# Kernel tuning notes

Measured on AMD Instinct MI355X. Metric: run time of the kernel, lower is better.

## Reference

```python
import jax, jax.numpy as jnp
from jax import lax
import numpy as np

DN = ('NCHW', 'OIHW', 'NCHW')

def _conv(x, w, b, s, p):
    out = lax.conv_general_dilated(x, w, (s, s), ((p, p), (p, p)), dimension_numbers=DN)
    return out + b[None, :, None, None]

def _convt(x, w, b):
    # torch ConvTranspose2d(k=3, stride=2, pad=1, out_pad=1) == lhs-dilated conv
    # with flipped kernel, pad (k-1-p, k-1-p+op) = (1, 2). Doubles H, W.
    wk = jnp.flip(w, (2, 3)).transpose(1, 0, 2, 3)  # [Cin,Cout,k,k] -> [Cout,Cin,k,k]
    out = lax.conv_general_dilated(x, wk, (1, 1), ((1, 2), (1, 2)), lhs_dilation=(2, 2), dimension_numbers=DN)
    return out + b[None, :, None, None]

def _bn(x, g, b):
    # training-mode batch stats over (N, H, W), eps=1e-5
    m = jnp.mean(x, (0, 2, 3), keepdims=True)
    v = jnp.var(x, (0, 2, 3), keepdims=True)
    return (x - m) * lax.rsqrt(v + 1e-5) * g[None, :, None, None] + b[None, :, None, None]

def _hsw(x):
    return x * jnp.clip(x + 3.0, 0.0, 6.0) * (1.0 / 6.0)

SCORE_THRESHOLD = 0.6
DOWN_SCALE = 4.0

def _forward(feature, ch_w1, ch_b1, ch_w2, ch_b2, ch_w3, ch_b3, ch_g1, ch_be1, ch_g2, ch_be2,
             cl_w1, cl_b1, cl_w2, cl_b2, cl_g, cl_be, cl_dw, cl_db,
             rg_tw, rg_tb, rg_g, rg_be, rg_w, rg_b, hm_tw, hm_tb):
    # ---- CommonHead (note: original reuses bn1 after both stride-2 convs) ----
    h = _bn(_conv(feature, ch_w1, ch_b1, 2, 1), ch_g1, ch_be1)   # [B,192,64,64]
    h = _bn(_conv(h, ch_w2, ch_b2, 2, 1), ch_g1, ch_be1)         # [B,192,32,32]
    h = _hsw(_bn(_conv(h, ch_w3, ch_b3, 1, 0), ch_g2, ch_be2))   # [B,32,32,32]
    # ---- PageClassifyNet ----
    c = _hsw(_bn(_conv(h, cl_w1, cl_b1, 1, 1), cl_g, cl_be))     # [B,32,32,32]
    c = _conv(c, cl_w2, cl_b2, 1, 1)                             # [B,1,32,32]
    cls = c.reshape(c.shape[0], -1) @ cl_dw.T + cl_db            # [B,2]
    r = _hsw(_bn(_convt(feature, rg_tw, rg_tb), rg_g, rg_be))    # [B,32,256,256]
    reg = _conv(r, rg_w, rg_b, 1, 1)                             # [B,2,256,256]
    # ---- AuxiliaryHeatmapNet ----
    hm = _convt(feature, hm_tw, hm_tb)                           # [B,8,256,256]
    # ---- keypoint decode (threshold + argmax + gather), vectorized over batch ----
    B, _, H, W = hm.shape
    flat = hm.transpose(0, 2, 3, 1).reshape(B, H * W, 8)          # HWC layout as in source
    pages = jnp.stack([flat[..., :4], flat[..., 4:]], axis=1)     # [B,2(pages),HW,4(corners)]
    idx = jnp.argmax(pages, axis=2)                               # [B,2,4] flat spatial index
    y_idx = (idx // W).astype(reg.dtype)
    x_idx = (idx % W).astype(reg.dtype)
    fi = idx.reshape(B, -1)                                       # [B,8]
    reg_flat = reg.reshape(B, 2, H * W)
    off_x = jnp.take_along_axis(reg_flat[:, 0, :], fi, axis=1).reshape(B, 2, 4)
    off_y = jnp.take_along_axis(reg_flat[:, 1, :], fi, axis=1).reshape(B, 2, 4)
    xs = jnp.clip((off_x + x_idx) * DOWN_SCALE / (W * DOWN_SCALE), 0.0, 1.0)
    ys = jnp.clip((off_y + y_idx) * DOWN_SCALE / (H * DOWN_SCALE), 0.0, 1.0)
    valid = cls > SCORE_THRESHOLD                                 # [B,2]
    label = jnp.broadcast_to(jnp.arange(2, dtype=xs.dtype)[None, :], (B, 2))
    row = jnp.concatenate([label[..., None], xs, ys], axis=-1)    # [B,2,9]
    return jnp.where(valid[..., None], row, jnp.asarray(-1.0, xs.dtype))


def setup_inputs() -> dict:
    key = jax.random.key(0)
    ks = jax.random.split(key, 32)
    rn = lambda k, shp, s=0.05: jax.random.normal(k, shp, dtype=jnp.float32) * s
    d = {}
    d['feature'] = jax.random.normal(ks[0], (8, 512, 128, 128), dtype=jnp.float32)
    d['ch_w1'] = rn(ks[1], (192, 512, 3, 3)); d['ch_b1'] = rn(ks[2], (192,))
    d['ch_w2'] = rn(ks[3], (192, 192, 3, 3)); d['ch_b2'] = rn(ks[4], (192,))
    d['ch_w3'] = rn(ks[5], (32, 192, 1, 1)); d['ch_b3'] = rn(ks[6], (32,))
    d['ch_g1'] = jnp.ones((192,), jnp.float32); d['ch_be1'] = jnp.zeros((192,), jnp.float32)
    d['ch_g2'] = jnp.ones((32,), jnp.float32); d['ch_be2'] = jnp.zeros((32,), jnp.float32)
    d['cl_w1'] = rn(ks[7], (32, 32, 3, 3)); d['cl_b1'] = rn(ks[8], (32,))
    d['cl_w2'] = rn(ks[9], (1, 32, 3, 3)); d['cl_b2'] = rn(ks[10], (1,))
    d['cl_g'] = jnp.ones((32,), jnp.float32); d['cl_be'] = jnp.zeros((32,), jnp.float32)
    d['cl_dw'] = rn(ks[11], (2, 1024), 0.1); d['cl_db'] = rn(ks[12], (2,))
    d['rg_tw'] = rn(ks[13], (512, 32, 3, 3)); d['rg_tb'] = rn(ks[14], (32,))
    d['rg_g'] = jnp.ones((32,), jnp.float32); d['rg_be'] = jnp.zeros((32,), jnp.float32)
    d['rg_w'] = rn(ks[15], (2, 32, 3, 3)); d['rg_b'] = rn(ks[16], (2,))
    d['hm_tw'] = rn(ks[17], (512, 8, 3, 3)); d['hm_tb'] = rn(ks[18], (8,))
    return d


def reference(feature, ch_w1, ch_b1, ch_w2, ch_b2, ch_w3, ch_b3, ch_g1, ch_be1, ch_g2, ch_be2,
              cl_w1, cl_b1, cl_w2, cl_b2, cl_g, cl_be, cl_dw, cl_db,
              rg_tw, rg_tb, rg_g, rg_be, rg_w, rg_b, hm_tw, hm_tb):
    return _forward(feature, ch_w1, ch_b1, ch_w2, ch_b2, ch_w3, ch_b3, ch_g1, ch_be1, ch_g2, ch_be2,
                    cl_w1, cl_b1, cl_w2, cl_b2, cl_g, cl_be, cl_dw, cl_db,
                    rg_tw, rg_tb, rg_g, rg_be, rg_w, rg_b, hm_tw, hm_tb)
```

## Files before the change

### kernel.cpp

```cpp
#include <hip/hip_runtime.h>

typedef unsigned short u16;
typedef u16 u16x8 __attribute__((ext_vector_type(8)));
typedef __bf16 bf16x8 __attribute__((ext_vector_type(8)));
typedef float f32x4 __attribute__((ext_vector_type(4)));

__device__ __forceinline__ float bf2f(u16 v) {
  unsigned u = ((unsigned)v) << 16;
  return __builtin_bit_cast(float, u);
}
__device__ __forceinline__ u16 f2bf(float f) {
  unsigned u = __builtin_bit_cast(unsigned, f);
  u += 0x7FFFu + ((u >> 16) & 1u);
  return (u16)(u >> 16);
}
__device__ __forceinline__ float hsw(float v) {
  return v * fminf(fmaxf(v + 3.f, 0.f), 6.f) * (1.f / 6.f);
}
__device__ __forceinline__ f32x4 mfma16(u16x8 a, u16x8 b, f32x4 c) {
  return __builtin_amdgcn_mfma_f32_16x16x32_bf16(
      __builtin_bit_cast(bf16x8, a), __builtin_bit_cast(bf16x8, b), c, 0, 0, 0);
}

#define LR 40

__global__ __launch_bounds__(256) void k_tobf(const float* __restrict__ f,
                                              u16* __restrict__ fbh) {
  __shared__ float tl[64 * 65];
  const int t = threadIdx.x;
  const int bid = blockIdx.x;
  const int ict = bid & 7, xt = (bid >> 3) & 1, y = (bid >> 4) & 127, n = bid >> 11;
  const int x0 = xt * 64, ic0 = ict * 64;
#pragma unroll
  for (int i = 0; i < 16; ++i) {
    const int e = t + i * 256;
    const int icl = e >> 6, xl = e & 63;
    tl[icl * 65 + xl] = f[((n * 512 + ic0 + icl) * 128 + y) * 128 + x0 + xl];
  }
  __syncthreads();
#pragma unroll
  for (int i = 0; i < 16; ++i) {
    const int e = t + i * 256;
    const int xl = e >> 6, icl = e & 63;
    const size_t idx = ((size_t)((n * 128 + y) * 128 + x0 + xl) << 9) + ic0 + icl;
    fbh[idx] = f2bf(tl[icl * 65 + xl]);
  }
}

__global__ __launch_bounds__(256) void k_pack1(const float* __restrict__ w,
                                               u16* __restrict__ bph) {
  const int e = blockIdx.x * 256 + threadIdx.x;
  const int ici = e & 31;
  const int rest = e >> 5;
  const int oc = rest % 192;
  const int kc = rest / 192;
  const int icc = kc & 15, tap = kc >> 4;
  const int ic = icc * 32 + ici;
  bph[e] = f2bf(w[(oc * 512 + ic) * 9 + tap]);
}

__global__ __launch_bounds__(256) void k_pack2(const float* __restrict__ w,
                                               u16* __restrict__ bph) {
  const int e = blockIdx.x * 256 + threadIdx.x;
  const int ici = e & 31;
  const int rest = e >> 5;
  const int oc = rest % 192;
  const int kc = rest / 192;
  const int icc = kc % 6, tap = kc / 6;
  const int ic = icc * 32 + ici;
  bph[e] = f2bf(w[(oc * 192 + ic) * 9 + tap]);
}

__global__ __launch_bounds__(256) void k_pack5(const float* __restrict__ rgw,
                                               const float* __restrict__ hmw,
                                               u16* __restrict__ bph) {
  const int e = blockIdx.x * 256 + threadIdx.x;
  const int ici = e & 31;
  const int rest = e >> 5;
  const int oc = rest % 48;
  const int sic = rest / 48;
  const int icc = sic & 15, slot = sic >> 4;
  const int ic = icc * 32 + ici;
  const int kytab[9] = {1, 1, 1, 2, 0, 2, 2, 0, 0};
  const int kxtab[9] = {1, 2, 0, 1, 1, 2, 0, 2, 0};
  const int ky = kytab[slot], kx = kxtab[slot];
  float v = 0.f;
  if (oc < 32)
    v = rgw[((ic * 32 + oc) * 3 + ky) * 3 + kx];
  else if (oc < 40)
    v = hmw[((ic * 8 + (oc - 32)) * 3 + ky) * 3 + kx];
  bph[e] = f2bf(v);
}

__global__ __launch_bounds__(256) void k_conv1(const u16* __restrict__ fbh,
                                               const u16* __restrict__ bph,
                                               const float* __restrict__ bias,
                                               float* __restrict__ y1) {
  __shared__ u16 Al[64 * LR];
  __shared__ u16 Bl[192 * LR];
  __shared__ float bl[192];
  const int t = threadIdx.x;
  const int n = blockIdx.x >> 6, oy = blockIdx.x & 63;
  if (t < 192) bl[t] = bias[t];
  const int lane = t & 63, wv = t >> 6;
  const int row = lane & 15, g = lane >> 4;
  const int oxs = t >> 2, icq = t & 3;
  const f32x4 z4 = {0.f, 0.f, 0.f, 0.f};
  f32x4 acc[4][3];
#pragma unroll
  for (int i = 0; i < 4; ++i)
#pragma unroll
    for (int j = 0; j < 3; ++j) acc[i][j] = z4;

  for (int kc = 0; kc < 144; ++kc) {
    const int tap = kc >> 4, icc = kc & 15;
    const int ky = tap / 3, kx = tap - ky * 3;
    const int iy = 2 * oy - 1 + ky;
    const int ix = 2 * oxs - 1 + kx;
    u16x8 av = {0, 0, 0, 0, 0, 0, 0, 0};
    if ((unsigned)iy < 128u && (unsigned)ix < 128u)
      av = *(const u16x8*)&fbh[((size_t)((n * 128 + iy) * 128 + ix) << 9) +
                               icc * 32 + icq * 8];
    u16x8 bv[3];
    const size_t bbase = (size_t)(tap * 16 + icc) * (192 * 32);
#pragma unroll
    for (int i = 0; i < 3; ++i) {
      const int e = t + i * 256;
      bv[i] = *(const u16x8*)&bph[bbase + (e >> 2) * 32 + (e & 3) * 8];
    }
    __syncthreads();
    *(u16x8*)&Al[oxs * LR + icq * 8] = av;
#pragma unroll
    for (int i = 0; i < 3; ++i) {
      const int e = t + i * 256;
      *(u16x8*)&Bl[(e >> 2) * LR + (e & 3) * 8] = bv[i];
    }
    __syncthreads();
    u16x8 af[4], bf[3];
#pragma unroll
    for (int mf = 0; mf < 4; ++mf)
      af[mf] = *(const u16x8*)&Al[(mf * 16 + row) * LR + g * 8];
#pragma unroll
    for (int nf = 0; nf < 3; ++nf)
      bf[nf] = *(const u16x8*)&Bl[(wv * 48 + nf * 16 + row) * LR + g * 8];
#pragma unroll
    for (int mf = 0; mf < 4; ++mf)
#pragma unroll
      for (int nf = 0; nf < 3; ++nf) acc[mf][nf] = mfma16(af[mf], bf[nf], acc[mf][nf]);
  }
#pragma unroll
  for (int mf = 0; mf < 4; ++mf)
#pragma unroll
    for (int nf = 0; nf < 3; ++nf)
#pragma unroll
      for (int r = 0; r < 4; ++r) {
        const int m = mf * 16 + g * 4 + r;
        const int oc = wv * 48 + nf * 16 + row;
        y1[((n * 64 + oy) * 64 + m) * 192 + oc] = acc[mf][nf][r] + bl[oc];
      }
}

__global__ __launch_bounds__(256) void k_conv2(const float* __restrict__ y1,
                                               const u16* __restrict__ bph,
                                               const float* __restrict__ bias,
                                               const float* __restrict__ sc,
                                               const float* __restrict__ sh,
                                               float* __restrict__ y2) {
  __shared__ u16 Al[64 * LR];
  __shared__ u16 Bl[192 * LR];
  __shared__ float bl[192], scl[192], shl[192];
  const int t = threadIdx.x;
  const int n = blockIdx.x >> 4, oyp = blockIdx.x & 15;
  if (t < 192) {
    bl[t] = bias[t];
    scl[t] = sc[t];
    shl[t] = sh[t];
  }
  __syncthreads();
  const int lane = t & 63, wv = t >> 6;
  const int row = lane & 15, g = lane >> 4;
  const int ms = t >> 2, icq = t & 3;
  const int ryr = ms >> 5, oxs = ms & 31;
  const f32x4 z4 = {0.f, 0.f, 0.f, 0.f};
  f32x4 acc[4][3];
#pragma unroll
  for (int i = 0; i < 4; ++i)
#pragma unroll
    for (int j = 0; j < 3; ++j) acc[i][j] = z4;

  for (int kc = 0; kc < 54; ++kc) {
    const int tap = kc / 6, icc = kc - tap * 6;
    const int ky = tap / 3, kx = tap - ky * 3;
    const int iy = 2 * (oyp * 2 + ryr) - 1 + ky;
    const int ix = 2 * oxs - 1 + kx;
    u16x8 av = {0, 0, 0, 0, 0, 0, 0, 0};
    if ((unsigned)iy < 64u && (unsigned)ix < 64u) {
      const int icb = icc * 32 + icq * 8;
      const float* base = &y1[((n * 64 + iy) * 64 + ix) * 192 + icb];
      const f32x4 r0 = *(const f32x4*)base;
      const f32x4 r1 = *(const f32x4*)(base + 4);
#pragma unroll
      for (int j = 0; j < 8; ++j) {
        const float r = (j < 4) ? r0[j & 3] : r1[j & 3];
        av[j] = f2bf(r * scl[icb + j] + shl[icb + j]);
      }
    }
    u16x8 bv[3];
    const size_t bbase = (size_t)(tap * 6 + icc) * (192 * 32);
#pragma unroll
    for (int i = 0; i < 3; ++i) {
      const int e = t + i * 256;
      bv[i] = *(const u16x8*)&bph[bbase + (e >> 2) * 32 + (e & 3) * 8];
    }
    __syncthreads();
    *(u16x8*)&Al[ms * LR + icq * 8] = av;
#pragma unroll
    for (int i = 0; i < 3; ++i) {
      const int e = t + i * 256;
      *(u16x8*)&Bl[(e >> 2) * LR + (e & 3) * 8] = bv[i];
    }
    __syncthreads();
    u16x8 af[4], bf[3];
#pragma unroll
    for (int mf = 0; mf < 4; ++mf)
      af[mf] = *(const u16x8*)&Al[(mf * 16 + row) * LR + g * 8];
#pragma unroll
    for (int nf = 0; nf < 3; ++nf)
      bf[nf] = *(const u16x8*)&Bl[(wv * 48 + nf * 16 + row) * LR + g * 8];
#pragma unroll
    for (int mf = 0; mf < 4; ++mf)
#pragma unroll
      for (int nf = 0; nf < 3; ++nf) acc[mf][nf] = mfma16(af[mf], bf[nf], acc[mf][nf]);
  }
#pragma unroll
  for (int mf = 0; mf < 4; ++mf)
#pragma unroll
    for (int nf = 0; nf < 3; ++nf)
#pragma unroll
      for (int r = 0; r < 4; ++r) {
        const int m = mf * 16 + g * 4 + r;
        const int oy = oyp * 2 + (m >> 5), ox = m & 31;
        const int oc = wv * 48 + nf * 16 + row;
        y2[((n * 32 + oy) * 32 + ox) * 192 + oc] = acc[mf][nf][r] + bl[oc];
      }
}

#define AST 40
#define ARS (130 * 40)
#define BST 40
__global__ __launch_bounds__(256) void k_convt(const u16* __restrict__ fbh,
                                               const u16* __restrict__ bph,
                                               const float* __restrict__ rgb,
                                               const float* __restrict__ hmb,
                                               u16* __restrict__ rr,
                                               float* __restrict__ hm) {
  __shared__ u16 AH[2 * ARS];
  __shared__ u16 BH[9 * 48 * BST];
  const int t = threadIdx.x;
  const int bid = (blockIdx.x & 7) * 128 + (blockIdx.x >> 3);
  const int n = bid >> 7, iyb = bid & 127;
  const int lane = t & 63, wv = t >> 6;
  const int row = lane & 15, g = lane >> 4;

  if (t < 8) {
    const int r = t >> 2, j = t & 3;
    const u16x8 z = {0, 0, 0, 0, 0, 0, 0, 0};
    *(u16x8*)&AH[r * ARS + 128 * AST + j * 8] = z;
  }

  float bias3[3];
#pragma unroll
  for (int nf = 0; nf < 3; ++nf) {
    const int oc = nf * 16 + row;
    bias3[nf] = (oc < 32) ? rgb[oc] : ((oc < 40) ? hmb[oc - 32] : 0.f);
  }

  const int SCt[9] = {0, 1, 1, 2, 2, 3, 3, 3, 3};
  const int SDt[9] = {0, 0, 0, 0, 1, 0, 0, 1, 1};
  const int SXt[9] = {0, 0, 1, 0, 0, 0, 1, 0, 1};

  int rr_[4], px_[4], iq_[4];
#pragma unroll
  for (int i = 0; i < 4; ++i) {
    const int u = t + i * 256;
    rr_[i] = u >> 9;
    px_[i] = (u >> 2) & 127;
    iq_[i] = u & 3;
  }

  const f32x4 z4 = {0.f, 0.f, 0.f, 0.f};
  f32x4 acc[4][2][3];
#pragma unroll
  for (int c = 0; c < 4; ++c)
#pragma unroll
    for (int m = 0; m < 2; ++m)
#pragma unroll
      for (int j = 0; j < 3; ++j) acc[c][m][j] = z4;

#define LOAD_A(ICC, DST)                                                       \
  _Pragma("unroll") for (int i = 0; i < 4; ++i) {                              \
    const int iy = iyb + rr_[i];                                               \
    u16x8 v = {0, 0, 0, 0, 0, 0, 0, 0};                                        \
    if (iy < 128)                                                              \
      v = *(const u16x8*)&fbh[((size_t)((n * 128 + iy) * 128 + px_[i]) << 9) + \
                              (ICC)*32 + iq_[i] * 8];                          \
    DST[i] = v;                                                                \
  }

#define LOAD_B(ICC, DST)                                                       \
  _Pragma("unroll") for (int i = 0; i < 7; ++i) {                              \
    const int e = t + i * 256;                                                 \
    u16x8 v = {0, 0, 0, 0, 0, 0, 0, 0};                                        \
    if (e < 1728) {                                                            \
      const int slot = e / 192, rem = e % 192;                                 \
      const int oc = rem >> 2, icq = rem & 3;                                  \
      v = *(const u16x8*)&bph[((size_t)((slot * 16 + (ICC)) * 48 + oc) << 5) + \
                              icq * 8];                                        \
    }                                                                          \
    DST[i] = v;                                                                \
  }

  u16x8 ahA[4], bhA[7], ahB[4], bhB[7];
  LOAD_A(0, ahA);
  LOAD_B(0, bhA);

  for (int icc = 0; icc < 16; ++icc) {
    __syncthreads();
#pragma unroll
    for (int i = 0; i < 4; ++i)
      *(u16x8*)&AH[rr_[i] * ARS + px_[i] * AST + iq_[i] * 8] = ahA[i];
#pragma unroll
    for (int i = 0; i < 7; ++i) {
      const int e = t + i * 256;
      if (e < 1728) {
        const int slot = e / 192, rem = e % 192;
        const int oc = rem >> 2, icq = rem & 3;
        *(u16x8*)&BH[(slot * 48 + oc) * BST + icq * 8] = bhA[i];
      }
    }
    __syncthreads();

    if (icc < 15) {
      LOAD_A(icc + 1, ahB);
      LOAD_B(icc + 1, bhB);
    }

#pragma unroll
    for (int slot = 0; slot < 9; ++slot) {
      const int cls = SCt[slot], diy = SDt[slot], dix = SXt[slot];
      const u16x8 bf0 = *(const u16x8*)&BH[(slot * 48 + row) * BST + g * 8];
      const u16x8 bf1 = *(const u16x8*)&BH[(slot * 48 + 16 + row) * BST + g * 8];
      const u16x8 bf2 = *(const u16x8*)&BH[(slot * 48 + 32 + row) * BST + g * 8];
#pragma unroll
      for (int mfl = 0; mfl < 2; ++mfl) {
        const int mf = wv * 2 + mfl;
        const u16x8 af =
            *(const u16x8*)&AH[diy * ARS + (mf * 16 + row + dix) * AST + g * 8];
        acc[cls][mfl][0] = mfma16(af, bf0, acc[cls][mfl][0]);
        acc[cls][mfl][1] = mfma16(af, bf1, acc[cls][mfl][1]);
        acc[cls][mfl][2] = mfma16(af, bf2, acc[cls][mfl][2]);
      }
    }

#pragma unroll
    for (int i = 0; i < 4; ++i) ahA[i] = ahB[i];
#pragma unroll
    for (int i = 0; i < 7; ++i) bhA[i] = bhB[i];
  }
#undef LOAD_A
#undef LOAD_B

#pragma unroll
  for (int cls = 0; cls < 4; ++cls) {
    const int oy = 2 * iyb + (cls >> 1);
    const int xp = cls & 1;
#pragma unroll
    for (int mfl = 0; mfl < 2; ++mfl)
#pragma unroll
      for (int nf = 0; nf < 3; ++nf)
#pragma unroll
        for (int r = 0; r < 4; ++r) {
          const int m = (wv * 2 + mfl) * 16 + g * 4 + r;
          const int ox = 2 * m + xp;
          const int oc = nf * 16 + row;
          const float v = acc[cls][mfl][nf][r] + bias3[nf];
          if (oc < 32)
            rr[((size_t)((n * 256 + oy) * 256 + ox)) * 32 + oc] = f2bf(v);
          else if (oc < 40)
            hm[(size_t)(n * 8 + (oc - 32)) * 65536 + oy * 256 + ox] = v;
        }
  }
}

template <int CG, bool BF16>
__global__ __launch_bounds__(256) void k_stats(const void* __restrict__ in_, int M,
                                               int PB, float* __restrict__ gsum,
                                               float* __restrict__ gsq) {
  const int C = CG * 32;
  __shared__ float red[8][CG * 32];
  const int t = threadIdx.x;
  const int pg = t >> 5, ln = t & 31;
  float s[CG], q[CG];
#pragma unroll
  for (int c = 0; c < CG; ++c) { s[c] = 0.f; q[c] = 0.f; }
  const int p0 = blockIdx.x * PB;
  const int pend = min(p0 + PB, M);
  for (int p = p0 + pg; p < pend; p += 8) {
#pragma unroll
    for (int c = 0; c < CG; ++c) {
      float v;
      if (BF16)
        v = bf2f(((const u16*)in_)[(size_t)p * C + c * 32 + ln]);
      else
        v = ((const float*)in_)[(size_t)p * C + c * 32 + ln];
      s[c] += v;
      q[c] += v * v;
    }
  }
#pragma unroll
  for (int c = 0; c < CG; ++c) red[pg][c * 32 + ln] = s[c];
  __syncthreads();
  if (t < C) {
    float tot = 0.f;
#pragma unroll
    for (int k = 0; k < 8; ++k) tot += red[k][t];
    atomicAdd(&gsum[t], tot);
  }
  __syncthreads();
#pragma unroll
  for (int c = 0; c < CG; ++c) red[pg][c * 32 + ln] = q[c];
  __syncthreads();
  if (t < C) {
    float tot = 0.f;
#pragma unroll
    for (int k = 0; k < 8; ++k) tot += red[k][t];
    atomicAdd(&gsq[t], tot);
  }
}

__global__ void k_bnfin(const float* __restrict__ gsum, const float* __restrict__ gsq,
                        const float* __restrict__ g, const float* __restrict__ be,
                        float invM, int C, float* __restrict__ sc,
                        float* __restrict__ sh) {
  const int t = threadIdx.x;
  if (t < C) {
    const float m = gsum[t] * invM;
    const float var = gsq[t] * invM - m * m;
    const float inv = rsqrtf(var + 1e-5f);
    const float s = g[t] * inv;
    sc[t] = s;
    sh[t] = be[t] - m * s;
  }
}

__global__ __launch_bounds__(256) void k_conv3(const float* __restrict__ y2,
                                               const float* __restrict__ w3,
                                               const float* __restrict__ b3,
                                               const float* __restrict__ sc,
                                               const float* __restrict__ sh,
                                               float* __restrict__ y3) {
  __shared__ float wl[32 * 192];
  __shared__ float scl[192], shl[192];
  const int t = threadIdx.x;
  for (int e = t; e < 6144; e += 256) wl[e] = w3[e];
  if (t < 192) {
    scl[t] = sc[t];
    shl[t] = sh[t];
  }
  __syncthreads();
  const int px = blockIdx.x * 256 + t;
  float acc[32];
#pragma unroll
  for (int oc = 0; oc < 32; ++oc) acc[oc] = 0.f;
  const float* base = &y2[(size_t)px * 192];
  for (int icb = 0; icb < 192; icb += 8) {
    const f32x4 r0 = *(const f32x4*)&base[icb];
    const f32x4 r1 = *(const f32x4*)&base[icb + 4];
    float v[8];
#pragma unroll
    for (int j = 0; j < 8; ++j) {
      const float r = (j < 4) ? r0[j & 3] : r1[j & 3];
      v[j] = r * scl[icb + j] + shl[icb + j];
    }
#pragma unroll
    for (int oc = 0; oc < 32; ++oc) {
      const f32x4 w0 = *(const f32x4*)&wl[oc * 192 + icb];
      const f32x4 w1 = *(const f32x4*)&wl[oc * 192 + icb + 4];
      acc[oc] += v[0] * w0[0] + v[1] * w0[1] + v[2] * w0[2] + v[3] * w0[3] +
                 v[4] * w1[0] + v[5] * w1[1] + v[6] * w1[2] + v[7] * w1[3];
    }
  }
#pragma unroll
  for (int oc = 0; oc < 32; ++oc) y3[(size_t)px * 32 + oc] = acc[oc] + b3[oc];
}

__global__ __launch_bounds__(256) void k_clsconv1(const float* __restrict__ y3,
                                                  const float* __restrict__ w1,
                                                  const float* __restrict__ b1,
                                                  const float* __restrict__ sc,
                                                  const float* __restrict__ sh,
                                                  float* __restrict__ c1) {
  __shared__ float wl[9216];
  __shared__ float scl[32], shl[32];
  const int t = threadIdx.x;
  for (int e = t; e < 9216; e += 256) {
    const int oc = e & 31;
    const int tmp = e >> 5;
    const int tap = tmp % 9, ic = tmp / 9;
    wl[e] = w1[(oc * 32 + ic) * 9 + tap];
  }
  if (t < 32) {
    scl[t] = sc[t];
    shl[t] = sh[t];
  }
  __syncthreads();
  const int px = blockIdx.x * 64 + (t & 63);
  const int ocg = t >> 6;
  const int n = px >> 10, y0 = (px >> 5) & 31, x0 = px & 31;
  float acc[8];
#pragma unroll
  for (int j = 0; j < 8; ++j) acc[j] = 0.f;
  for (int tap = 0; tap < 9; ++tap) {
    const int dy = tap / 3 - 1, dx = tap % 3 - 1;
    const int yy = y0 + dy, xx = x0 + dx;
    if ((unsigned)yy < 32u && (unsigned)xx < 32u) {
      const float* ib = &y3[((n << 10) + yy * 32 + xx) * 32];
      for (int ic = 0; ic < 32; ++ic) {
        const float v = hsw(ib[ic] * scl[ic] + shl[ic]);
        const float* wp = &wl[(ic * 9 + tap) * 32 + ocg * 8];
#pragma unroll
        for (int j = 0; j < 8; ++j) acc[j] += v * wp[j];
      }
    }
  }
#pragma unroll
  for (int j = 0; j < 8; ++j) c1[px * 32 + ocg * 8 + j] = acc[j] + b1[ocg * 8 + j];
}

__global__ __launch_bounds__(256) void k_cls(const float* __restrict__ c1,
                                             const float* __restrict__ w2,
                                             const float* __restrict__ b2,
                                             const float* __restrict__ dw,
                                             const float* __restrict__ db,
                                             const float* __restrict__ sc,
                                             const float* __restrict__ sh,
                                             float* __restrict__ cls) {
  __shared__ float wl[288];
  __shared__ float scl[32], shl[32];
  __shared__ float red0[256], red1[256];
  const int t = threadIdx.x;
  const int n = blockIdx.x;
  for (int e = t; e < 288; e += 256) wl[e] = w2[e];
  if (t < 32) {
    scl[t] = sc[t];
    shl[t] = sh[t];
  }
  __syncthreads();
  float s0 = 0.f, s1 = 0.f;
  for (int i = 0; i < 4; ++i) {
    const int px = i * 256 + t;
    const int y0 = px >> 5, x0 = px & 31;
    float c2 = b2[0];
    for (int tap = 0; tap < 9; ++tap) {
      const int dy = tap / 3 - 1, dx = tap % 3 - 1;
      const int yy = y0 + dy, xx = x0 + dx;
      if ((unsigned)yy < 32u && (unsigned)xx < 32u) {
        const float* ib = &c1[((n << 10) + yy * 32 + xx) * 32];
        for (int ic = 0; ic < 32; ++ic)
          c2 += hsw(ib[ic] * scl[ic] + shl[ic]) * wl[ic * 9 + tap];
      }
    }
    s0 += c2 * dw[px];
    s1 += c2 * dw[1024 + px];
  }
  red0[t] = s0;
  red1[t] = s1;
  __syncthreads();
  for (int s = 128; s; s >>= 1) {
    if (t < s) {
      red0[t] += red0[t + s];
      red1[t] += red1[t + s];
    }
    __syncthreads();
  }
  if (t == 0) {
    cls[n * 2 + 0] = red0[0] + db[0];
    cls[n * 2 + 1] = red1[0] + db[1];
  }
}

__global__ __launch_bounds__(256) void k_regconv(const u16* __restrict__ rr,
                                                 const float* __restrict__ w,
                                                 const float* __restrict__ b,
                                                 const float* __restrict__ sc,
                                                 const float* __restrict__ sh,
                                                 float* __restrict__ reg) {
  __shared__ u16 rl[3 * 258 * 33];
  __shared__ float wl[576];
  __shared__ float scl[32], shl[32];
  const int t = threadIdx.x;
  const int n = blockIdx.x >> 8, oy = blockIdx.x & 255;
  for (int e = t; e < 576; e += 256) wl[e] = w[e];
  if (t < 32) {
    scl[t] = sc[t];
    shl[t] = sh[t];
  }
  if (t < 192) {
    const int ry = t / 64, side = (t >> 5) & 1, ic = t & 31;
    rl[(ry * 258 + side * 257) * 33 + ic] = 0;
  }
  __syncthreads();
  for (int e = t; e < 3072; e += 256) {
    const int icq8 = e & 3;
    const int pxx = (e >> 2) & 255;
    const int ry = e >> 10;
    const int rowi = oy - 1 + ry;
    u16x8 raw = {0, 0, 0, 0, 0, 0, 0, 0};
    bool ok = (unsigned)rowi < 256u;
    if (ok)
      raw = *(const u16x8*)&rr[((size_t)((n * 256 + rowi) * 256 + pxx)) * 32 + icq8 * 8];
#pragma unroll
    for (int j = 0; j < 8; ++j) {
      const int ic = icq8 * 8 + j;
      float v = 0.f;
      if (ok) v = hsw(bf2f(raw[j]) * scl[ic] + shl[ic]);
      rl[(ry * 258 + pxx + 1) * 33 + ic] = f2bf(v);
    }
  }
  __syncthreads();
  const int px = t;
  float a0 = b[0], a1 = b[1];
#pragma unroll
  for (int ry = 0; ry < 3; ++ry)
#pragma unroll
    for (int kx = 0; kx < 3; ++kx) {
      const u16* ib = &rl[(ry * 258 + px + kx) * 33];
      for (int ic = 0; ic < 32; ++ic) {
        const float v = bf2f(ib[ic]);
        a0 += v * wl[ic * 9 + ry * 3 + kx];
        a1 += v * wl[288 + ic * 9 + ry * 3 + kx];
      }
    }
  reg[(n * 2 + 0) * 65536 + oy * 256 + px] = a0;
  reg[(n * 2 + 1) * 65536 + oy * 256 + px] = a1;
}

__global__ __launch_bounds__(256) void k_argmax(const float* __restrict__ hm,
                                                int* __restrict__ idx) {
  __shared__ float bv[256];
  __shared__ int bi[256];
  const int t = threadIdx.x;
  const float* base = &hm[(size_t)blockIdx.x * 65536];
  float best = -3.402823466e38f;
  int bidx = 2147483647;
  for (int i = t; i < 65536; i += 256) {
    const float v = base[i];
    if (v > best) {
      best = v;
      bidx = i;
    }
  }
  bv[t] = best;
  bi[t] = bidx;
  __syncthreads();
  for (int s = 128; s; s >>= 1) {
    if (t < s) {
      if (bv[t + s] > bv[t] || (bv[t + s] == bv[t] && bi[t + s] < bi[t])) {
        bv[t] = bv[t + s];
        bi[t] = bi[t + s];
      }
    }
    __syncthreads();
  }
  if (t == 0) idx[blockIdx.x] = bi[0];
}

__global__ void k_final(const float* __restrict__ cls, const int* __restrict__ idx,
                        const float* __restrict__ reg, float* __restrict__ out) {
  const int t = threadIdx.x;
  if (t >= 16) return;
  const int n = t >> 1, p = t & 1;
  const float cv = cls[n * 2 + p];
  float* o = &out[(n * 2 + p) * 9];
  if (!(cv > 0.6f)) {
    for (int i = 0; i < 9; ++i) o[i] = -1.f;
    return;
  }
  o[0] = (float)p;
  for (int c = 0; c < 4; ++c) {
    const int id = idx[n * 8 + p * 4 + c];
    const int yi = id >> 8, xi = id & 255;
    const float ox_ = reg[(n * 2 + 0) * 65536 + id];
    const float oy_ = reg[(n * 2 + 1) * 65536 + id];
    o[1 + c] = fminf(fmaxf((ox_ + (float)xi) * (1.f / 256.f), 0.f), 1.f);
    o[5 + c] = fminf(fmaxf((oy_ + (float)yi) * (1.f / 256.f), 0.f), 1.f);
  }
}

extern "C" void kernel_launch(void* const* d_in, const int* in_sizes, int n_in,
                              void* d_out, int out_size, void* d_ws, size_t ws_size,
                              hipStream_t stream) {
  const float* feature = (const float*)d_in[0];
  const float* ch_w1 = (const float*)d_in[1];
  const float* ch_b1 = (const float*)d_in[2];
  const float* ch_w2 = (const float*)d_in[3];
  const float* ch_b2 = (const float*)d_in[4];
  const float* ch_w3 = (const float*)d_in[5];
  const float* ch_b3 = (const float*)d_in[6];
  const float* ch_g1 = (const float*)d_in[7];
  const float* ch_be1 = (const float*)d_in[8];
  const float* ch_g2 = (const float*)d_in[9];
  const float* ch_be2 = (const float*)d_in[10];
  const float* cl_w1 = (const float*)d_in[11];
  const float* cl_b1 = (const float*)d_in[12];
  const float* cl_w2 = (const float*)d_in[13];
  const float* cl_b2 = (const float*)d_in[14];
  const float* cl_g = (const float*)d_in[15];
  const float* cl_be = (const float*)d_in[16];
  const float* cl_dw = (const float*)d_in[17];
  const float* cl_db = (const float*)d_in[18];
  const float* rg_tw = (const float*)d_in[19];
  const float* rg_tb = (const float*)d_in[20];
  const float* rg_g = (const float*)d_in[21];
  const float* rg_be = (const float*)d_in[22];
  const float* rg_w = (const float*)d_in[23];
  const float* rg_b = (const float*)d_in[24];
  const float* hm_tw = (const float*)d_in[25];
  const float* hm_tb = (const float*)d_in[26];
  float* out = (float*)d_out;

  char* w = (char*)d_ws;
  const size_t OFF_FB = 0;
  const size_t OFF_BP1 = 134217728;
  const size_t OFF_BP2 = 135987200;
  const size_t OFF_BP5 = 136650752;
  const size_t OFF_Y1 = 137093120;
  const size_t OFF_Y2 = 162258944;
  const size_t OFF_Y3 = 168550400;
  const size_t OFF_C1 = 169598976;
  const size_t OFF_RR = 170647552;
  const size_t OFF_HM = 204201984;
  const size_t OFF_REG = 220979200;
  const size_t OFF_STATS = 225173504;
  const size_t OFF_PARAMS = 225177344;
  const size_t OFF_CLS = 225181184;
  const size_t OFF_IDX = 225181248;
  const size_t WS_NEED = 225181504;
  if (ws_size < WS_NEED) return;

  u16* FB = (u16*)(w + OFF_FB);
  u16* BP1 = (u16*)(w + OFF_BP1);
  u16* BP2 = (u16*)(w + OFF_BP2);
  u16* BP5 = (u16*)(w + OFF_BP5);
  float* Y1 = (float*)(w + OFF_Y1);
  float* Y2 = (float*)(w + OFF_Y2);
  float* Y3 = (float*)(w + OFF_Y3);
  float* C1 = (float*)(w + OFF_C1);
  u16* RR = (u16*)(w + OFF_RR);
  float* HM = (float*)(w + OFF_HM);
  float* REG = (float*)(w + OFF_REG);
  float* GSUM = (float*)(w + OFF_STATS);
  float* GSQ = GSUM + 480;
  float* SC = (float*)(w + OFF_PARAMS);
  float* SH = SC + 480;
  float* CLS = (float*)(w + OFF_CLS);
  int* IDX = (int*)(w + OFF_IDX);

  (void)hipMemsetAsync(w + OFF_STATS, 0, 3840, stream);

  k_tobf<<<16384, 256, 0, stream>>>(feature, FB);
  k_pack1<<<3456, 256, 0, stream>>>(ch_w1, BP1);
  k_pack2<<<1296, 256, 0, stream>>>(ch_w2, BP2);
  k_pack5<<<864, 256, 0, stream>>>(rg_tw, hm_tw, BP5);

  k_conv1<<<512, 256, 0, stream>>>(FB, BP1, ch_b1, Y1);
  k_stats<6, false><<<128, 256, 0, stream>>>(Y1, 32768, 256, GSUM + 0, GSQ + 0);
  k_bnfin<<<1, 256, 0, stream>>>(GSUM + 0, GSQ + 0, ch_g1, ch_be1, 1.f / 32768.f, 192,
                                 SC + 0, SH + 0);
  k_conv2<<<128, 256, 0, stream>>>(Y1, BP2, ch_b2, SC + 0, SH + 0, Y2);
  k_stats<6, false><<<32, 256, 0, stream>>>(Y2, 8192, 256, GSUM + 192, GSQ + 192);
  k_bnfin<<<1, 256, 0, stream>>>(GSUM + 192, GSQ + 192, ch_g1, ch_be1, 1.f / 8192.f,
                                 192, SC + 192, SH + 192);
  k_conv3<<<32, 256, 0, stream>>>(Y2, ch_w3, ch_b3, SC + 192, SH + 192, Y3);
  k_stats<1, false><<<8, 256, 0, stream>>>(Y3, 8192, 1024, GSUM + 384, GSQ + 384);
  k_bnfin<<<1, 256, 0, stream>>>(GSUM + 384, GSQ + 384, ch_g2, ch_be2, 1.f / 8192.f,
                                 32, SC + 384, SH + 384);
  k_clsconv1<<<128, 256, 0, stream>>>(Y3, cl_w1, cl_b1, SC + 384, SH + 384, C1);
  k_stats<1, false><<<8, 256, 0, stream>>>(C1, 8192, 1024, GSUM + 416, GSQ + 416);
  k_bnfin<<<1, 256, 0, stream>>>(GSUM + 416, GSQ + 416, cl_g, cl_be, 1.f / 8192.f, 32,
                                 SC + 416, SH + 416);
  k_cls<<<8, 256, 0, stream>>>(C1, cl_w2, cl_b2, cl_dw, cl_db, SC + 416, SH + 416,
                               CLS);
  k_convt<<<1024, 256, 0, stream>>>(FB, BP5, rg_tb, hm_tb, RR, HM);
  k_stats<1, true><<<256, 256, 0, stream>>>(RR, 524288, 2048, GSUM + 448, GSQ + 448);
  k_bnfin<<<1, 256, 0, stream>>>(GSUM + 448, GSQ + 448, rg_g, rg_be, 1.f / 524288.f,
                                 32, SC + 448, SH + 448);
  k_regconv<<<2048, 256, 0, stream>>>(RR, rg_w, rg_b, SC + 448, SH + 448, REG);
  k_argmax<<<64, 256, 0, stream>>>(HM, IDX);
  k_final<<<1, 64, 0, stream>>>(CLS, IDX, REG, out);
}
```

Before: 836.3 us.

## Prefetch next K-chunk in conv1/conv2, store Y1 as bf16, retune convt LDS

conv1 and conv2 now issue global loads for the next K-chunk into registers before running the MFMAs on the current chunk, so load latency overlaps compute. The conv1 output Y1 is stored as bf16 instead of fp32, which halves its write and read traffic in conv1, the stats pass and conv2. The convt kernel drops the LDS row padding from 40 to 32 elements and hoists its A-fragment loads out of the slot loop. In exchange, the unpadded stride may cause LDS bank conflicts, the extra registers may lower occupancy, and BN statistics are now computed on bf16-rounded values.

```diff
diff --git a/kernel.cpp b/kernel.cpp
--- a/kernel.cpp
+++ b/kernel.cpp
@@ -95,7 +95,7 @@
 __global__ __launch_bounds__(256) void k_conv1(const u16* __restrict__ fbh,
                                                const u16* __restrict__ bph,
                                                const float* __restrict__ bias,
-                                               float* __restrict__ y1) {
+                                               u16* __restrict__ y1) {
   __shared__ u16 Al[64 * LR];
   __shared__ u16 Bl[192 * LR];
   __shared__ float bl[192];
@@ -112,30 +112,37 @@
 #pragma unroll
     for (int j = 0; j < 3; ++j) acc[i][j] = z4;
 
+#define C1_LOAD(KC, AV, BV)                                                    \
+  {                                                                            \
+    const int tap_ = (KC) >> 4, icc_ = (KC)&15;                                \
+    const int ky_ = tap_ / 3, kx_ = tap_ - ky_ * 3;                            \
+    const int iy_ = 2 * oy - 1 + ky_;                                          \
+    const int ix_ = 2 * oxs - 1 + kx_;                                         \
+    u16x8 v_ = {0, 0, 0, 0, 0, 0, 0, 0};                                       \
+    if ((unsigned)iy_ < 128u && (unsigned)ix_ < 128u)                          \
+      v_ = *(const u16x8*)&fbh[((size_t)((n * 128 + iy_) * 128 + ix_) << 9) +  \
+                               icc_ * 32 + icq * 8];                           \
+    AV = v_;                                                                   \
+    const size_t bbase_ = (size_t)(tap_ * 16 + icc_) * (192 * 32);             \
+    _Pragma("unroll") for (int i_ = 0; i_ < 3; ++i_) {                         \
+      const int e_ = t + i_ * 256;                                             \
+      BV[i_] = *(const u16x8*)&bph[bbase_ + (e_ >> 2) * 32 + (e_ & 3) * 8];    \
+    }                                                                          \
+  }
+
+  u16x8 avA, bvA[3], avB, bvB[3];
+  C1_LOAD(0, avA, bvA);
+
   for (int kc = 0; kc < 144; ++kc) {
-    const int tap = kc >> 4, icc = kc & 15;
-    const int ky = tap / 3, kx = tap - ky * 3;
-    const int iy = 2 * oy - 1 + ky;
-    const int ix = 2 * oxs - 1 + kx;
-    u16x8 av = {0, 0, 0, 0, 0, 0, 0, 0};
-    if ((unsigned)iy < 128u && (unsigned)ix < 128u)
-      av = *(const u16x8*)&fbh[((size_t)((n * 128 + iy) * 128 + ix) << 9) +
-                               icc * 32 + icq * 8];
-    u16x8 bv[3];
-    const size_t bbase = (size_t)(tap * 16 + icc) * (192 * 32);
+    __syncthreads();
+    *(u16x8*)&Al[oxs * LR + icq * 8] = avA;
 #pragma unroll
     for (int i = 0; i < 3; ++i) {
       const int e = t + i * 256;
-      bv[i] = *(const u16x8*)&bph[bbase + (e >> 2) * 32 + (e & 3) * 8];
+      *(u16x8*)&Bl[(e >> 2) * LR + (e & 3) * 8] = bvA[i];
     }
     __syncthreads();
-    *(u16x8*)&Al[oxs * LR + icq * 8] = av;
-#pragma unroll
-    for (int i = 0; i < 3; ++i) {
-      const int e = t + i * 256;
-      *(u16x8*)&Bl[(e >> 2) * LR + (e & 3) * 8] = bv[i];
-    }
-    __syncthreads();
+    if (kc < 143) C1_LOAD(kc + 1, avB, bvB);
     u16x8 af[4], bf[3];
 #pragma unroll
     for (int mf = 0; mf < 4; ++mf)
@@ -147,7 +154,11 @@
     for (int mf = 0; mf < 4; ++mf)
 #pragma unroll
       for (int nf = 0; nf < 3; ++nf) acc[mf][nf] = mfma16(af[mf], bf[nf], acc[mf][nf]);
-  }
+    avA = avB;
+#pragma unroll
+    for (int i = 0; i < 3; ++i) bvA[i] = bvB[i];
+  }
+#undef C1_LOAD
 #pragma unroll
   for (int mf = 0; mf < 4; ++mf)
 #pragma unroll
@@ -156,11 +167,11 @@
       for (int r = 0; r < 4; ++r) {
         const int m = mf * 16 + g * 4 + r;
         const int oc = wv * 48 + nf * 16 + row;
-        y1[((n * 64 + oy) * 64 + m) * 192 + oc] = acc[mf][nf][r] + bl[oc];
+        y1[((n * 64 + oy) * 64 + m) * 192 + oc] = f2bf(acc[mf][nf][r] + bl[oc]);
       }
 }
 
-__global__ __launch_bounds__(256) void k_conv2(const float* __restrict__ y1,
+__global__ __launch_bounds__(256) void k_conv2(const u16* __restrict__ y1,
                                                const u16* __restrict__ bph,
                                                const float* __restrict__ bias,
                                                const float* __restrict__ sc,
@@ -188,38 +199,47 @@
 #pragma unroll
     for (int j = 0; j < 3; ++j) acc[i][j] = z4;
 
+#define C2_LOAD(KC, RAW, OK, BV)                                               \
+  {                                                                            \
+    const int tap_ = (KC) / 6, icc_ = (KC)-tap_ * 6;                           \
+    const int ky_ = tap_ / 3, kx_ = tap_ - ky_ * 3;                            \
+    const int iy_ = 2 * (oyp * 2 + ryr) - 1 + ky_;                             \
+    const int ix_ = 2 * oxs - 1 + kx_;                                         \
+    OK = ((unsigned)iy_ < 64u) && ((unsigned)ix_ < 64u);                       \
+    u16x8 v_ = {0, 0, 0, 0, 0, 0, 0, 0};                                       \
+    if (OK)                                                                    \
+      v_ = *(const u16x8*)&y1[((n * 64 + iy_) * 64 + ix_) * 192 + icc_ * 32 +  \
+                              icq * 8];                                        \
+    RAW = v_;                                                                  \
+    const size_t bbase_ = (size_t)(tap_ * 6 + icc_) * (192 * 32);              \
+    _Pragma("unroll") for (int i_ = 0; i_ < 3; ++i_) {                         \
+      const int e_ = t + i_ * 256;                                             \
+      BV[i_] = *(const u16x8*)&bph[bbase_ + (e_ >> 2) * 32 + (e_ & 3) * 8];    \
+    }                                                                          \
+  }
+
+  u16x8 rawA, bvA[3], rawB, bvB[3];
+  bool okA, okB;
+  C2_LOAD(0, rawA, okA, bvA);
+
   for (int kc = 0; kc < 54; ++kc) {
     const int tap = kc / 6, icc = kc - tap * 6;
-    const int ky = tap / 3, kx = tap - ky * 3;
-    const int iy = 2 * (oyp * 2 + ryr) - 1 + ky;
-    const int ix = 2 * oxs - 1 + kx;
+    const int icb = icc * 32 + icq * 8;
     u16x8 av = {0, 0, 0, 0, 0, 0, 0, 0};
-    if ((unsigned)iy < 64u && (unsigned)ix < 64u) {
-      const int icb = icc * 32 + icq * 8;
-      const float* base = &y1[((n * 64 + iy) * 64 + ix) * 192 + icb];
-      const f32x4 r0 = *(const f32x4*)base;
-      const f32x4 r1 = *(const f32x4*)(base + 4);
-#pragma unroll
-      for (int j = 0; j < 8; ++j) {
-        const float r = (j < 4) ? r0[j & 3] : r1[j & 3];
-        av[j] = f2bf(r * scl[icb + j] + shl[icb + j]);
-      }
-    }
-    u16x8 bv[3];
-    const size_t bbase = (size_t)(tap * 6 + icc) * (192 * 32);
+    if (okA) {
+#pragma unroll
+      for (int j = 0; j < 8; ++j)
+        av[j] = f2bf(bf2f(rawA[j]) * scl[icb + j] + shl[icb + j]);
+    }
+    __syncthreads();
+    *(u16x8*)&Al[ms * LR + icq * 8] = av;
 #pragma unroll
     for (int i = 0; i < 3; ++i) {
       const int e = t + i * 256;
-      bv[i] = *(const u16x8*)&bph[bbase + (e >> 2) * 32 + (e & 3) * 8];
+      *(u16x8*)&Bl[(e >> 2) * LR + (e & 3) * 8] = bvA[i];
     }
     __syncthreads();
-    *(u16x8*)&Al[ms * LR + icq * 8] = av;
-#pragma unroll
-    for (int i = 0; i < 3; ++i) {
-      const int e = t + i * 256;
-      *(u16x8*)&Bl[(e >> 2) * LR + (e & 3) * 8] = bv[i];
-    }
-    __syncthreads();
+    if (kc < 53) C2_LOAD(kc + 1, rawB, okB, bvB);
     u16x8 af[4], bf[3];
 #pragma unroll
     for (int mf = 0; mf < 4; ++mf)
@@ -231,7 +251,12 @@
     for (int mf = 0; mf < 4; ++mf)
 #pragma unroll
       for (int nf = 0; nf < 3; ++nf) acc[mf][nf] = mfma16(af[mf], bf[nf], acc[mf][nf]);
-  }
+    rawA = rawB;
+    okA = okB;
+#pragma unroll
+    for (int i = 0; i < 3; ++i) bvA[i] = bvB[i];
+  }
+#undef C2_LOAD
 #pragma unroll
   for (int mf = 0; mf < 4; ++mf)
 #pragma unroll
@@ -245,17 +270,16 @@
       }
 }
 
-#define AST 40
-#define ARS (130 * 40)
-#define BST 40
+#define AST2 32
+#define ARS2 (129 * 32)
 __global__ __launch_bounds__(256) void k_convt(const u16* __restrict__ fbh,
                                                const u16* __restrict__ bph,
                                                const float* __restrict__ rgb,
                                                const float* __restrict__ hmb,
                                                u16* __restrict__ rr,
                                                float* __restrict__ hm) {
-  __shared__ u16 AH[2 * ARS];
-  __shared__ u16 BH[9 * 48 * BST];
+  __shared__ u16 AH[2 * ARS2];
+  __shared__ u16 BH[9 * 48 * 32];
   const int t = threadIdx.x;
   const int bid = (blockIdx.x & 7) * 128 + (blockIdx.x >> 3);
   const int n = bid >> 7, iyb = bid & 127;
@@ -265,7 +289,7 @@
   if (t < 8) {
     const int r = t >> 2, j = t & 3;
     const u16x8 z = {0, 0, 0, 0, 0, 0, 0, 0};
-    *(u16x8*)&AH[r * ARS + 128 * AST + j * 8] = z;
+    *(u16x8*)&AH[r * ARS2 + 128 * AST2 + j * 8] = z;
   }
 
   float bias3[3];
@@ -328,14 +352,14 @@
     __syncthreads();
 #pragma unroll
     for (int i = 0; i < 4; ++i)
-      *(u16x8*)&AH[rr_[i] * ARS + px_[i] * AST + iq_[i] * 8] = ahA[i];
+      *(u16x8*)&AH[rr_[i] * ARS2 + px_[i] * AST2 + iq_[i] * 8] = ahA[i];
 #pragma unroll
     for (int i = 0; i < 7; ++i) {
       const int e = t + i * 256;
       if (e < 1728) {
         const int slot = e / 192, rem = e % 192;
         const int oc = rem >> 2, icq = rem & 3;
-        *(u16x8*)&BH[(slot * 48 + oc) * BST + icq * 8] = bhA[i];
+        *(u16x8*)&BH[(slot * 48 + oc) * AST2 + icq * 8] = bhA[i];
       }
     }
     __syncthreads();
@@ -345,17 +369,26 @@
       LOAD_B(icc + 1, bhB);
     }
 
+    u16x8 afr[2][2][2];
+#pragma unroll
+    for (int diy = 0; diy < 2; ++diy)
+#pragma unroll
+      for (int mfl = 0; mfl < 2; ++mfl)
+#pragma unroll
+        for (int dix = 0; dix < 2; ++dix)
+          afr[diy][mfl][dix] =
+              *(const u16x8*)&AH[diy * ARS2 +
+                                 ((wv * 2 + mfl) * 16 + row + dix) * AST2 + g * 8];
+
 #pragma unroll
     for (int slot = 0; slot < 9; ++slot) {
       const int cls = SCt[slot], diy = SDt[slot], dix = SXt[slot];
-      const u16x8 bf0 = *(const u16x8*)&BH[(slot * 48 + row) * BST + g * 8];
-      const u16x8 bf1 = *(const u16x8*)&BH[(slot * 48 + 16 + row) * BST + g * 8];
-      const u16x8 bf2 = *(const u16x8*)&BH[(slot * 48 + 32 + row) * BST + g * 8];
+      const u16x8 bf0 = *(const u16x8*)&BH[(slot * 48 + row) * AST2 + g * 8];
+      const u16x8 bf1 = *(const u16x8*)&BH[(slot * 48 + 16 + row) * AST2 + g * 8];
+      const u16x8 bf2 = *(const u16x8*)&BH[(slot * 48 + 32 + row) * AST2 + g * 8];
 #pragma unroll
       for (int mfl = 0; mfl < 2; ++mfl) {
-        const int mf = wv * 2 + mfl;
-        const u16x8 af =
-            *(const u16x8*)&AH[diy * ARS + (mf * 16 + row + dix) * AST + g * 8];
+        const u16x8 af = afr[diy][mfl][dix];
         acc[cls][mfl][0] = mfma16(af, bf0, acc[cls][mfl][0]);
         acc[cls][mfl][1] = mfma16(af, bf1, acc[cls][mfl][1]);
         acc[cls][mfl][2] = mfma16(af, bf2, acc[cls][mfl][2]);
@@ -735,24 +768,24 @@
   const size_t OFF_BP2 = 135987200;
   const size_t OFF_BP5 = 136650752;
   const size_t OFF_Y1 = 137093120;
-  const size_t OFF_Y2 = 162258944;
-  const size_t OFF_Y3 = 168550400;
-  const size_t OFF_C1 = 169598976;
-  const size_t OFF_RR = 170647552;
-  const size_t OFF_HM = 204201984;
-  const size_t OFF_REG = 220979200;
-  const size_t OFF_STATS = 225173504;
-  const size_t OFF_PARAMS = 225177344;
-  const size_t OFF_CLS = 225181184;
-  const size_t OFF_IDX = 225181248;
-  const size_t WS_NEED = 225181504;
+  const size_t OFF_Y2 = 149676032;
+  const size_t OFF_Y3 = 155967488;
+  const size_t OFF_C1 = 157016064;
+  const size_t OFF_RR = 158064640;
+  const size_t OFF_HM = 191619072;
+  const size_t OFF_REG = 208396288;
+  const size_t OFF_STATS = 212590592;
+  const size_t OFF_PARAMS = 212594432;
+  const size_t OFF_CLS = 212598272;
+  const size_t OFF_IDX = 212598336;
+  const size_t WS_NEED = 212598592;
   if (ws_size < WS_NEED) return;
 
   u16* FB = (u16*)(w + OFF_FB);
   u16* BP1 = (u16*)(w + OFF_BP1);
   u16* BP2 = (u16*)(w + OFF_BP2);
   u16* BP5 = (u16*)(w + OFF_BP5);
-  float* Y1 = (float*)(w + OFF_Y1);
+  u16* Y1 = (u16*)(w + OFF_Y1);
   float* Y2 = (float*)(w + OFF_Y2);
   float* Y3 = (float*)(w + OFF_Y3);
   float* C1 = (float*)(w + OFF_C1);
@@ -774,7 +807,7 @@
   k_pack5<<<864, 256, 0, stream>>>(rg_tw, hm_tw, BP5);
 
   k_conv1<<<512, 256, 0, stream>>>(FB, BP1, ch_b1, Y1);
-  k_stats<6, false><<<128, 256, 0, stream>>>(Y1, 32768, 256, GSUM + 0, GSQ + 0);
+  k_stats<6, true><<<128, 256, 0, stream>>>(Y1, 32768, 256, GSUM + 0, GSQ + 0);
   k_bnfin<<<1, 256, 0, stream>>>(GSUM + 0, GSQ + 0, ch_g1, ch_be1, 1.f / 32768.f, 192,
                                  SC + 0, SH + 0);
   k_conv2<<<128, 256, 0, stream>>>(Y1, BP2, ch_b2, SC + 0, SH + 0, Y2);
```

New measurement: 849.5 us. About the same (+1.6%).
